# Kernel tuning notes

Measured on AMD Instinct MI355X. Metric: run time of the kernel, lower is better.

The kernel has to match this reference:

```python
import jax, jax.numpy as jnp
import numpy as np

DEPTH = 11          # tree depth
D = 1024            # input_width
H = 32              # hidden_width (leaf MLP)
O = 1024            # output_width
B = 4096            # flattened token batch
N_LEAVES = 2 ** DEPTH
N_NODES = 2 ** DEPTH - 1


def setup_inputs() -> dict:
    key = jax.random.key(0)
    ks = jax.random.split(key, 7)
    f1 = 1.0 / np.sqrt(D)
    f2 = 1.0 / np.sqrt(H)
    u = lambda k, shape, f: jax.random.uniform(k, shape, jnp.float32, -f, f)
    return {
        "x": jax.random.normal(ks[0], (B, D), jnp.float32),
        "node_weights": u(ks[1], (N_NODES, D), f1),
        "node_biases": u(ks[2], (N_NODES,), f1),   # (n_nodes,1) in torch; flattened
        "w1s": u(ks[3], (N_LEAVES, D, H), f1),
        "b1s": u(ks[4], (N_LEAVES, H), f1),
        "w2s": u(ks[5], (N_LEAVES, H, O), f2),
        "b2s": u(ks[6], (N_LEAVES, O), f2),
    }


def reference(x, node_weights, node_biases, w1s, b1s, w2s, b2s):
    # --- hard tree descent (eval_forward) ---
    nodes = jnp.zeros((x.shape[0],), jnp.int32)
    for i in range(DEPTH):  # fixed small loop over tree depth
        w = node_weights[nodes]                       # [B, D] gathered plane coeffs
        b = node_biases[nodes]                        # [B]
        score = jnp.einsum('bd,bd->b', x, w) + b      # per-sample dot product
        choice = (score >= 0).astype(jnp.int32)
        platform = 2 ** i - 1
        next_platform = 2 ** (i + 1) - 1
        nodes = (nodes - platform) * 2 + choice + next_platform
    leaves = nodes - (2 ** DEPTH - 1)                 # [B] leaf index per sample

    # --- per-sample leaf MLP with gathered weights ---
    h = jax.nn.relu(jnp.einsum('bd,bdh->bh', x, w1s[leaves]) + b1s[leaves])  # [B, H]
    out = jnp.einsum('bh,bho->bo', h, w2s[leaves]) + b2s[leaves]             # [B, O]
    return out
```

## Files before the change

kernel.cpp:

```cpp
#include <hip/hip_runtime.h>

#define DEPTH 11
#define D 1024
#define H 32
#define OW 1024
#define B 4096
#define N_LEAVES 2048
#define N_NODES 2047
#define SMAX 4
#define MAX_ITEMS 3072
#define NBLK 512
#define MAXK 6

typedef __attribute__((address_space(3))) void lds_void;
typedef const __attribute__((address_space(1))) void glb_void;

#define SB __builtin_amdgcn_sched_barrier(0)
#define WAITV(N) do { asm volatile("s_waitcnt vmcnt(" #N ")" ::: "memory"); SB; } while (0)
#define WAITLG0  do { asm volatile("s_waitcnt lgkmcnt(0)" ::: "memory"); SB; } while (0)
#define BARRIER  do { WAITLG0; __builtin_amdgcn_s_barrier(); \
                      asm volatile("" ::: "memory"); SB; } while (0)

__global__ __launch_bounds__(256) void descent_kernel(
    const float* __restrict__ x, const float* __restrict__ nw,
    const float* __restrict__ nb, int* __restrict__ leaf,
    int* __restrict__ rnk, int* __restrict__ count)
{
    int lane = threadIdx.x & 63;
    int wv   = threadIdx.x >> 6;
    int samp = blockIdx.x * 4 + wv;

    const float4* xp = (const float4*)(x + (size_t)samp * D);
    float4 xf[4];
#pragma unroll
    for (int k = 0; k < 4; k++) xf[k] = xp[lane + 64 * k];

    int node = 0;
#pragma unroll
    for (int i = 0; i < DEPTH; i++) {
        const float4* wp = (const float4*)(nw + (size_t)node * D);
        double s = 0.0;
#pragma unroll
        for (int k = 0; k < 4; k++) {
            float4 wf = wp[lane + 64 * k];
            s += (double)xf[k].x * (double)wf.x;
            s += (double)xf[k].y * (double)wf.y;
            s += (double)xf[k].z * (double)wf.z;
            s += (double)xf[k].w * (double)wf.w;
        }
#pragma unroll
        for (int m = 32; m >= 1; m >>= 1) s += __shfl_xor(s, m, 64);
        double score = s + (double)nb[node];
        int choice = (score >= 0.0) ? 1 : 0;
        node = 2 * node + 1 + choice;
    }
    int lf = node - N_NODES;
    if (lane == 0) {
        leaf[samp] = lf;
        rnk[samp]  = atomicAdd(&count[lf], 1);
    }
}

__global__ __launch_bounds__(256) void scan_kernel(
    const int* __restrict__ count, int* __restrict__ offsets)
{
    __shared__ int tot[256];
    int t = threadIdx.x;
    int c[8], s = 0;
#pragma unroll
    for (int k = 0; k < 8; k++) { c[k] = count[t * 8 + k]; s += c[k]; }
    tot[t] = s;
    __syncthreads();
    for (int off = 1; off < 256; off <<= 1) {
        int v = (t >= off) ? tot[t - off] : 0;
        __syncthreads();
        tot[t] += v;
        __syncthreads();
    }
    int base = (t > 0) ? tot[t - 1] : 0;
#pragma unroll
    for (int k = 0; k < 8; k++) { offsets[t * 8 + k] = base; base += c[k]; }
}

__global__ __launch_bounds__(256) void scatter_kernel(
    const int* __restrict__ leaf, const int* __restrict__ rnk,
    const int* __restrict__ offsets, int* __restrict__ bucket)
{
    int i = blockIdx.x * 256 + threadIdx.x;
    bucket[offsets[leaf[i]] + rnk[i]] = i;
}

__global__ __launch_bounds__(256) void build_items_kernel(
    const int* __restrict__ count, int* __restrict__ items,
    int* __restrict__ nitems)
{
    int l = blockIdx.x * 256 + threadIdx.x;
    int c = count[l];
    if (c > 0) {
        int k = (c + SMAX - 1) / SMAX;
        int base = atomicAdd(nitems, k);
        for (int i = 0; i < k; i++)
            items[base + i] = l | ((i * SMAX) << 11);
    }
}

__device__ __forceinline__ void stage4(const float* src, float* dst, int lane)
{
#pragma unroll
    for (int i = 0; i < 4; i++)
        __builtin_amdgcn_global_load_lds((glb_void*)(src + i * 256 + lane * 4),
                                         (lds_void*)(dst + i * 256), 16, 0, 0);
}

__device__ __forceinline__ void stageL2g(const float* w2w, int cj, float* dst, int lane)
{
#pragma unroll
    for (int jl = 0; jl < 4; jl++)
        __builtin_amdgcn_global_load_lds(
            (glb_void*)(w2w + (size_t)(cj * 4 + jl) * OW + lane * 4),
            (lds_void*)(dst + jl * 256), 16, 0, 0);
}

__device__ __forceinline__ void stageXB(const float* x, const int* sid4,
                                        const float* b1, const float* b2,
                                        float* xsd, float* b1d, float* b2d,
                                        int wave, int lane)
{
#pragma unroll
    for (int s = 0; s < 4; s++)
        __builtin_amdgcn_global_load_lds(
            (glb_void*)(x + (size_t)sid4[s] * D + wave * 256 + lane * 4),
            (lds_void*)(xsd + s * D + wave * 256), 16, 0, 0);
    __builtin_amdgcn_global_load_lds(
        (glb_void*)(b1 + ((lane < 32) ? lane : 31)), (lds_void*)b1d, 4, 0, 0);
    __builtin_amdgcn_global_load_lds(
        (glb_void*)(b2 + wave * 256 + lane * 4), (lds_void*)b2d, 16, 0, 0);
}

__device__ __forceinline__ void l1c(const float* p, const float* xsw, int c,
                                    int lane, int dg, float4* acc)
{
#pragma unroll
    for (int u = 0; u < 4; u++) {
        float4 w = ((const float4*)p)[u * 64 + lane];
#pragma unroll
        for (int s = 0; s < 4; s++) {
            float xv = xsw[s * D + c * 32 + u * 8 + dg];
            acc[s].x += xv * w.x;
            acc[s].y += xv * w.y;
            acc[s].z += xv * w.z;
            acc[s].w += xv * w.w;
        }
    }
}

__device__ __forceinline__ void l2c(const float* p, const float (*hsv)[32], int cj,
                                    int lane, float4* o)
{
#pragma unroll
    for (int jl = 0; jl < 4; jl++) {
        float4 w = ((const float4*)p)[jl * 64 + lane];
#pragma unroll
        for (int s = 0; s < 4; s++) {
            float hv = hsv[s][cj * 4 + jl];
            o[s].x += hv * w.x;
            o[s].y += hv * w.y;
            o[s].z += hv * w.z;
            o[s].w += hv * w.w;
        }
    }
}

__global__ __launch_bounds__(256, 2) void mlp_kernel(
    const float* __restrict__ x, const float* __restrict__ w1s,
    const float* __restrict__ b1s, const float* __restrict__ w2s,
    const float* __restrict__ b2s, const int* __restrict__ offsets,
    const int* __restrict__ count, const int* __restrict__ bucket,
    const int* __restrict__ items, const int* __restrict__ nitems,
    float* __restrict__ out)
{
    __shared__ float xs[SMAX * D];
    __shared__ float wq_[4][2][1024];
    __shared__ float pl1[4][SMAX][32];
    __shared__ float hs[SMAX][32];
    __shared__ float b1l[2][4][64];
    __shared__ float b2l[2][4][256];
    __shared__ int   md_leaf[MAXK];
    __shared__ int   md_sid[MAXK][4];

    const int tid = threadIdx.x, lane = tid & 63, wave = tid >> 6;
    const int dg = lane >> 3;
    const int bid = blockIdx.x;

    int nit = nitems[0];
    if (tid < MAXK) {
        int idx = bid + tid * NBLK;
        if (idx < nit) {
            int it = items[idx];
            int l = it & (N_LEAVES - 1), st = it >> 11;
            int c = count[l] - st;
            int S = (c < SMAX) ? c : SMAX;
            int off = offsets[l] + st;
            md_leaf[tid] = l;
            for (int s = 0; s < 4; s++)
                md_sid[tid][s] = bucket[off + ((s < S) ? s : (S - 1))];
        }
    }
    __syncthreads();
    int n_my = (nit - bid + NBLK - 1) >> 9;
    if (n_my <= 0) return;
    if (n_my > MAXK) n_my = MAXK;

    float* WQ0 = &wq_[wave][0][0];
    float* WQ1 = &wq_[wave][1][0];
    const float* xsw = xs + wave * 256;

    int lc = md_leaf[0];
    {
        const float* w1w = w1s + (size_t)lc * 32768 + wave * 8192;
        stage4(w1w, WQ0, lane);
        stageXB(x, md_sid[0], b1s + lc * H, b2s + (size_t)lc * OW,
                xs, &b1l[0][wave][0], &b2l[0][wave][0], wave, lane);
        stage4(w1w + 1024, WQ1, lane);
        stage4(w1w + 1024, WQ1, lane);
    }

    for (int k = 0; k < n_my; k++) {
        const int p  = k & 1;
        const int kn = (k + 1 < n_my) ? (k + 1) : k;
        const int ln = md_leaf[kn];
        const float* w1c = w1s + (size_t)lc * 32768 + wave * 8192;
        const float* w2c = w2s + (size_t)lc * 32768 + wave * 256;
        const float* w1n = w1s + (size_t)ln * 32768 + wave * 8192;
        int sc[4];
#pragma unroll
        for (int s = 0; s < 4; s++) sc[s] = md_sid[k][s];

        float4 acc[4];
#pragma unroll
        for (int s = 0; s < 4; s++) acc[s] = make_float4(0.f, 0.f, 0.f, 0.f);

        WAITV(8);  l1c(WQ0, xsw, 0, lane, dg, acc); SB; stage4(w1c + 2 * 1024, WQ0, lane);
        WAITV(8);  l1c(WQ1, xsw, 1, lane, dg, acc); SB; stage4(w1c + 3 * 1024, WQ1, lane);
        WAITV(4);  l1c(WQ0, xsw, 2, lane, dg, acc); SB; stage4(w1c + 4 * 1024, WQ0, lane);
        WAITV(4);  l1c(WQ1, xsw, 3, lane, dg, acc); SB; stage4(w1c + 5 * 1024, WQ1, lane);
        WAITV(4);  l1c(WQ0, xsw, 4, lane, dg, acc); SB; stage4(w1c + 6 * 1024, WQ0, lane);
        WAITV(4);  l1c(WQ1, xsw, 5, lane, dg, acc); SB; stage4(w1c + 7 * 1024, WQ1, lane);
        WAITV(4);  l1c(WQ0, xsw, 6, lane, dg, acc); SB; stageL2g(w2c, 0, WQ0, lane);
        WAITV(4);  l1c(WQ1, xsw, 7, lane, dg, acc); SB; stageL2g(w2c, 1, WQ1, lane);

#pragma unroll
        for (int m = 8; m <= 32; m <<= 1)
#pragma unroll
            for (int s = 0; s < 4; s++) {
                acc[s].x += __shfl_xor(acc[s].x, m, 64);
                acc[s].y += __shfl_xor(acc[s].y, m, 64);
                acc[s].z += __shfl_xor(acc[s].z, m, 64);
                acc[s].w += __shfl_xor(acc[s].w, m, 64);
            }
        if (dg == 0) {
#pragma unroll
            for (int s = 0; s < 4; s++)
                *(float4*)&pl1[wave][s][(lane & 7) * 4] = acc[s];
        }
        BARRIER;
        if (tid < 128) {
            int s2 = tid >> 5, j2 = tid & 31;
            float sum = pl1[0][s2][j2] + pl1[1][s2][j2] + pl1[2][s2][j2] +
                        pl1[3][s2][j2] + b1l[p][tid >> 6][j2];
            hs[s2][j2] = fmaxf(sum, 0.f);
        }
        BARRIER;

        float4 o[4];
#pragma unroll
        for (int s = 0; s < 4; s++) o[s] = make_float4(0.f, 0.f, 0.f, 0.f);

        WAITV(4);  l2c(WQ0, hs, 0, lane, o); SB; stageL2g(w2c, 2, WQ0, lane);
        WAITV(4);  l2c(WQ1, hs, 1, lane, o); SB; stageL2g(w2c, 3, WQ1, lane);
        WAITV(4);  l2c(WQ0, hs, 2, lane, o); SB; stageL2g(w2c, 4, WQ0, lane);
        WAITV(4);  l2c(WQ1, hs, 3, lane, o); SB; stageL2g(w2c, 5, WQ1, lane);
        WAITV(4);  l2c(WQ0, hs, 4, lane, o); SB; stageL2g(w2c, 6, WQ0, lane);
        WAITV(4);  l2c(WQ1, hs, 5, lane, o); SB; stageL2g(w2c, 7, WQ1, lane);
        WAITV(4);  l2c(WQ0, hs, 6, lane, o); SB;
        stage4(w1n, WQ0, lane);
        stageXB(x, md_sid[kn], b1s + ln * H, b2s + (size_t)ln * OW,
                xs, &b1l[p ^ 1][wave][0], &b2l[p ^ 1][wave][0], wave, lane);
        WAITV(10); l2c(WQ1, hs, 7, lane, o); SB;
        stage4(w1n + 1024, WQ1, lane);

        float4 bv = ((const float4*)&b2l[p][wave][0])[lane];
#pragma unroll
        for (int s = 0; s < 4; s++) {
            float4 o4;
            o4.x = o[s].x + bv.x;
            o4.y = o[s].y + bv.y;
            o4.z = o[s].z + bv.z;
            o4.w = o[s].w + bv.w;
            *(float4*)(out + (size_t)sc[s] * OW + wave * 256 + lane * 4) = o4;
        }
        lc = ln;
    }
}

extern "C" void kernel_launch(void* const* d_in, const int* in_sizes, int n_in,
                              void* d_out, int out_size, void* d_ws, size_t ws_size,
                              hipStream_t stream)
{
    const float* x   = (const float*)d_in[0];
    const float* nw  = (const float*)d_in[1];
    const float* nb  = (const float*)d_in[2];
    const float* w1s = (const float*)d_in[3];
    const float* b1s = (const float*)d_in[4];
    const float* w2s = (const float*)d_in[5];
    const float* b2s = (const float*)d_in[6];
    float* out = (float*)d_out;

    int* leaf    = (int*)d_ws;
    int* rnk     = leaf + B;
    int* count   = rnk + B;
    int* offsets = count + N_LEAVES;
    int* bucket  = offsets + N_LEAVES;
    int* items   = bucket + B;
    int* nitems  = items + MAX_ITEMS;

    hipMemsetAsync(count, 0, N_LEAVES * sizeof(int), stream);
    hipMemsetAsync(nitems, 0, sizeof(int), stream);
    descent_kernel<<<B / 4, 256, 0, stream>>>(x, nw, nb, leaf, rnk, count);
    scan_kernel<<<1, 256, 0, stream>>>(count, offsets);
    scatter_kernel<<<B / 256, 256, 0, stream>>>(leaf, rnk, offsets, bucket);
    build_items_kernel<<<N_LEAVES / 256, 256, 0, stream>>>(count, items, nitems);
    mlp_kernel<<<NBLK, 256, 0, stream>>>(x, w1s, b1s, w2s, b2s,
                                         offsets, count, bucket,
                                         items, nitems, out);
}
```

Measured before the change: 129.8 us.

## Stream leaf MLP weights into registers instead of LDS staging, raise occupancy

Replaces the LDS double-buffered staging of W1/W2 tiles (global_load_lds) with direct global_load_dwordx4 into register arrays under manual vmcnt-based pipelining, and removes the per-wave weight LDS buffers. It also raises the launch bound to 3 blocks per CU and changes the work split to 768 blocks with at most 4 items each. The aim is to cut LDS traffic and ds_read latency and to increase occupancy for this memory-bound gathered-weight MLP. The cost is much higher register pressure from 24 float4 buffers, which under the new launch bound could cause spills, and the hand-counted vmcnt waits are fragile.

Measured after the change: 128.1 us. No clear change (-1.3%).

```diff
diff --git a/kernel.cpp b/kernel.cpp
--- a/kernel.cpp
+++ b/kernel.cpp
@@ -9,9 +9,10 @@
 #define N_NODES 2047
 #define SMAX 4
 #define MAX_ITEMS 3072
-#define NBLK 512
-#define MAXK 6
-
+#define NBLK 768
+#define MAXK 4
+
+typedef float f32x4 __attribute__((ext_vector_type(4)));
 typedef __attribute__((address_space(3))) void lds_void;
 typedef const __attribute__((address_space(1))) void glb_void;
 
@@ -20,6 +21,8 @@
 #define WAITLG0  do { asm volatile("s_waitcnt lgkmcnt(0)" ::: "memory"); SB; } while (0)
 #define BARRIER  do { WAITLG0; __builtin_amdgcn_s_barrier(); \
                       asm volatile("" ::: "memory"); SB; } while (0)
+#define GLOAD(dst, ptr) \
+    asm volatile("global_load_dwordx4 %0, %1, off" : "=&v"(dst) : "v"(ptr) : "memory")
 
 __global__ __launch_bounds__(256) void descent_kernel(
     const float* __restrict__ x, const float* __restrict__ nw,
@@ -104,74 +107,7 @@
     }
 }
 
-__device__ __forceinline__ void stage4(const float* src, float* dst, int lane)
-{
-#pragma unroll
-    for (int i = 0; i < 4; i++)
-        __builtin_amdgcn_global_load_lds((glb_void*)(src + i * 256 + lane * 4),
-                                         (lds_void*)(dst + i * 256), 16, 0, 0);
-}
-
-__device__ __forceinline__ void stageL2g(const float* w2w, int cj, float* dst, int lane)
-{
-#pragma unroll
-    for (int jl = 0; jl < 4; jl++)
-        __builtin_amdgcn_global_load_lds(
-            (glb_void*)(w2w + (size_t)(cj * 4 + jl) * OW + lane * 4),
-            (lds_void*)(dst + jl * 256), 16, 0, 0);
-}
-
-__device__ __forceinline__ void stageXB(const float* x, const int* sid4,
-                                        const float* b1, const float* b2,
-                                        float* xsd, float* b1d, float* b2d,
-                                        int wave, int lane)
-{
-#pragma unroll
-    for (int s = 0; s < 4; s++)
-        __builtin_amdgcn_global_load_lds(
-            (glb_void*)(x + (size_t)sid4[s] * D + wave * 256 + lane * 4),
-            (lds_void*)(xsd + s * D + wave * 256), 16, 0, 0);
-    __builtin_amdgcn_global_load_lds(
-        (glb_void*)(b1 + ((lane < 32) ? lane : 31)), (lds_void*)b1d, 4, 0, 0);
-    __builtin_amdgcn_global_load_lds(
-        (glb_void*)(b2 + wave * 256 + lane * 4), (lds_void*)b2d, 16, 0, 0);
-}
-
-__device__ __forceinline__ void l1c(const float* p, const float* xsw, int c,
-                                    int lane, int dg, float4* acc)
-{
-#pragma unroll
-    for (int u = 0; u < 4; u++) {
-        float4 w = ((const float4*)p)[u * 64 + lane];
-#pragma unroll
-        for (int s = 0; s < 4; s++) {
-            float xv = xsw[s * D + c * 32 + u * 8 + dg];
-            acc[s].x += xv * w.x;
-            acc[s].y += xv * w.y;
-            acc[s].z += xv * w.z;
-            acc[s].w += xv * w.w;
-        }
-    }
-}
-
-__device__ __forceinline__ void l2c(const float* p, const float (*hsv)[32], int cj,
-                                    int lane, float4* o)
-{
-#pragma unroll
-    for (int jl = 0; jl < 4; jl++) {
-        float4 w = ((const float4*)p)[jl * 64 + lane];
-#pragma unroll
-        for (int s = 0; s < 4; s++) {
-            float hv = hsv[s][cj * 4 + jl];
-            o[s].x += hv * w.x;
-            o[s].y += hv * w.y;
-            o[s].z += hv * w.z;
-            o[s].w += hv * w.w;
-        }
-    }
-}
-
-__global__ __launch_bounds__(256, 2) void mlp_kernel(
+__global__ __launch_bounds__(256, 3) void mlp_kernel(
     const float* __restrict__ x, const float* __restrict__ w1s,
     const float* __restrict__ b1s, const float* __restrict__ w2s,
     const float* __restrict__ b2s, const int* __restrict__ offsets,
@@ -179,17 +115,16 @@
     const int* __restrict__ items, const int* __restrict__ nitems,
     float* __restrict__ out)
 {
-    __shared__ float xs[SMAX * D];
-    __shared__ float wq_[4][2][1024];
-    __shared__ float pl1[4][SMAX][32];
-    __shared__ float hs[SMAX][32];
-    __shared__ float b1l[2][4][64];
-    __shared__ float b2l[2][4][256];
-    __shared__ int   md_leaf[MAXK];
-    __shared__ int   md_sid[MAXK][4];
+    __shared__ __align__(16) float xs[SMAX][D];
+    __shared__ __align__(16) float pl1[4][SMAX][32];
+    __shared__ __align__(16) float hs[SMAX][32];
+    __shared__ __align__(16) float b1l[2][4][64];
+    __shared__ __align__(16) float b2l[2][4][256];
+    __shared__ int md_leaf[MAXK];
+    __shared__ int md_sid[MAXK][4];
 
     const int tid = threadIdx.x, lane = tid & 63, wave = tid >> 6;
-    const int dg = lane >> 3;
+    const int dg = lane >> 3, lane4 = lane * 4;
     const int bid = blockIdx.x;
 
     int nit = nitems[0];
@@ -207,61 +142,78 @@
         }
     }
     __syncthreads();
-    int n_my = (nit - bid + NBLK - 1) >> 9;
-    if (n_my <= 0) return;
+    if (bid >= nit) return;
+    int n_my = (nit - bid + NBLK - 1) / NBLK;
     if (n_my > MAXK) n_my = MAXK;
 
-    float* WQ0 = &wq_[wave][0][0];
-    float* WQ1 = &wq_[wave][1][0];
-    const float* xsw = xs + wave * 256;
+    f32x4 w1r[2][4];
+    f32x4 w2r[16];
+
+#define L1I(base, cc, bb) do { _Pragma("unroll") \
+    for (int u = 0; u < 4; u++) \
+        GLOAD(w1r[bb][u], (base) + (cc) * 1024 + u * 256 + lane4); } while (0)
+
+#define L1C(cc, bb) do { _Pragma("unroll") \
+    for (int u = 0; u < 4; u++) { \
+        f32x4 wv_ = w1r[bb][u]; \
+        _Pragma("unroll") \
+        for (int s = 0; s < 4; s++) \
+            acc[s] += xs[s][wave * 256 + (cc) * 32 + u * 8 + dg] * wv_; } } while (0)
 
     int lc = md_leaf[0];
+    const float* w1x = w1s + (size_t)lc * 32768 + wave * 8192;
     {
-        const float* w1w = w1s + (size_t)lc * 32768 + wave * 8192;
-        stage4(w1w, WQ0, lane);
-        stageXB(x, md_sid[0], b1s + lc * H, b2s + (size_t)lc * OW,
-                xs, &b1l[0][wave][0], &b2l[0][wave][0], wave, lane);
-        stage4(w1w + 1024, WQ1, lane);
-        stage4(w1w + 1024, WQ1, lane);
+#pragma unroll
+        for (int pp = 0; pp < 4; pp++)
+            __builtin_amdgcn_global_load_lds(
+                (glb_void*)(x + (size_t)md_sid[0][pp] * D + wave * 256 + lane4),
+                (lds_void*)(&xs[pp][wave * 256]), 16, 0, 0);
+        __builtin_amdgcn_global_load_lds(
+            (glb_void*)(b1s + lc * H + ((lane < 32) ? lane : 31)),
+            (lds_void*)(&b1l[0][wave][0]), 4, 0, 0);
+        __builtin_amdgcn_global_load_lds(
+            (glb_void*)(b2s + (size_t)lc * OW + wave * 256 + lane4),
+            (lds_void*)(&b2l[0][wave][0]), 16, 0, 0);
+        L1I(w1x, 0, 0); L1I(w1x, 1, 1);
+        L1I(w1x, 0, 0); L1I(w1x, 1, 1);
     }
 
     for (int k = 0; k < n_my; k++) {
-        const int p  = k & 1;
-        const int kn = (k + 1 < n_my) ? (k + 1) : k;
+        const int p  = k & 1, pn = p ^ 1;
+        const int kn = (k + 1 < n_my) ? k + 1 : k;
         const int ln = md_leaf[kn];
-        const float* w1c = w1s + (size_t)lc * 32768 + wave * 8192;
-        const float* w2c = w2s + (size_t)lc * 32768 + wave * 256;
+        const float* w2x = w2s + (size_t)lc * 32768 + wave * 256;
         const float* w1n = w1s + (size_t)ln * 32768 + wave * 8192;
-        int sc[4];
-#pragma unroll
-        for (int s = 0; s < 4; s++) sc[s] = md_sid[k][s];
-
-        float4 acc[4];
-#pragma unroll
-        for (int s = 0; s < 4; s++) acc[s] = make_float4(0.f, 0.f, 0.f, 0.f);
-
-        WAITV(8);  l1c(WQ0, xsw, 0, lane, dg, acc); SB; stage4(w1c + 2 * 1024, WQ0, lane);
-        WAITV(8);  l1c(WQ1, xsw, 1, lane, dg, acc); SB; stage4(w1c + 3 * 1024, WQ1, lane);
-        WAITV(4);  l1c(WQ0, xsw, 2, lane, dg, acc); SB; stage4(w1c + 4 * 1024, WQ0, lane);
-        WAITV(4);  l1c(WQ1, xsw, 3, lane, dg, acc); SB; stage4(w1c + 5 * 1024, WQ1, lane);
-        WAITV(4);  l1c(WQ0, xsw, 4, lane, dg, acc); SB; stage4(w1c + 6 * 1024, WQ0, lane);
-        WAITV(4);  l1c(WQ1, xsw, 5, lane, dg, acc); SB; stage4(w1c + 7 * 1024, WQ1, lane);
-        WAITV(4);  l1c(WQ0, xsw, 6, lane, dg, acc); SB; stageL2g(w2c, 0, WQ0, lane);
-        WAITV(4);  l1c(WQ1, xsw, 7, lane, dg, acc); SB; stageL2g(w2c, 1, WQ1, lane);
+        int sidc[4];
+#pragma unroll
+        for (int s = 0; s < 4; s++) sidc[s] = md_sid[k][s];
+
+        f32x4 acc[4] = {};
+
+        WAITV(8); L1C(0, 0); L1I(w1x, 2, 0);
+        WAITV(8); L1C(1, 1); L1I(w1x, 3, 1);
+        WAITV(4); L1C(2, 0); L1I(w1x, 4, 0);
+        WAITV(4); L1C(3, 1); L1I(w1x, 5, 1);
+        WAITV(4); L1C(4, 0); L1I(w1x, 6, 0);
+        WAITV(4); L1C(5, 1); L1I(w1x, 7, 1);
+        WAITV(4); L1C(6, 0);
+#pragma unroll
+        for (int j = 0; j < 8; j++) GLOAD(w2r[j], w2x + j * 1024 + lane4);
+        WAITV(8); L1C(7, 1);
+#pragma unroll
+        for (int j = 8; j < 16; j++) GLOAD(w2r[j], w2x + j * 1024 + lane4);
 
 #pragma unroll
         for (int m = 8; m <= 32; m <<= 1)
 #pragma unroll
-            for (int s = 0; s < 4; s++) {
-                acc[s].x += __shfl_xor(acc[s].x, m, 64);
-                acc[s].y += __shfl_xor(acc[s].y, m, 64);
-                acc[s].z += __shfl_xor(acc[s].z, m, 64);
-                acc[s].w += __shfl_xor(acc[s].w, m, 64);
-            }
+            for (int s = 0; s < 4; s++)
+#pragma unroll
+                for (int e = 0; e < 4; e++)
+                    acc[s][e] += __shfl_xor(acc[s][e], m, 64);
         if (dg == 0) {
 #pragma unroll
             for (int s = 0; s < 4; s++)
-                *(float4*)&pl1[wave][s][(lane & 7) * 4] = acc[s];
+                *(f32x4*)&pl1[wave][s][(lane & 7) * 4] = acc[s];
         }
         BARRIER;
         if (tid < 128) {
@@ -272,35 +224,46 @@
         }
         BARRIER;
 
-        float4 o[4];
-#pragma unroll
-        for (int s = 0; s < 4; s++) o[s] = make_float4(0.f, 0.f, 0.f, 0.f);
-
-        WAITV(4);  l2c(WQ0, hs, 0, lane, o); SB; stageL2g(w2c, 2, WQ0, lane);
-        WAITV(4);  l2c(WQ1, hs, 1, lane, o); SB; stageL2g(w2c, 3, WQ1, lane);
-        WAITV(4);  l2c(WQ0, hs, 2, lane, o); SB; stageL2g(w2c, 4, WQ0, lane);
-        WAITV(4);  l2c(WQ1, hs, 3, lane, o); SB; stageL2g(w2c, 5, WQ1, lane);
-        WAITV(4);  l2c(WQ0, hs, 4, lane, o); SB; stageL2g(w2c, 6, WQ0, lane);
-        WAITV(4);  l2c(WQ1, hs, 5, lane, o); SB; stageL2g(w2c, 7, WQ1, lane);
-        WAITV(4);  l2c(WQ0, hs, 6, lane, o); SB;
-        stage4(w1n, WQ0, lane);
-        stageXB(x, md_sid[kn], b1s + ln * H, b2s + (size_t)ln * OW,
-                xs, &b1l[p ^ 1][wave][0], &b2l[p ^ 1][wave][0], wave, lane);
-        WAITV(10); l2c(WQ1, hs, 7, lane, o); SB;
-        stage4(w1n + 1024, WQ1, lane);
-
-        float4 bv = ((const float4*)&b2l[p][wave][0])[lane];
+        f32x4 o[4] = {};
+#pragma unroll
+        for (int jj = 0; jj < 32; jj++) {
+            if (jj == 31) { WAITV(14); } else { WAITV(15); }
+            f32x4 w = w2r[jj & 15];
+#pragma unroll
+            for (int s = 0; s < 4; s++) o[s] += hs[s][jj] * w;
+            if (jj < 16) {
+                GLOAD(w2r[jj & 15], w2x + (jj + 16) * 1024 + lane4);
+            } else if (jj < 20) {
+                const int pp = jj - 16;
+                __builtin_amdgcn_global_load_lds(
+                    (glb_void*)(x + (size_t)md_sid[kn][pp] * D + wave * 256 + lane4),
+                    (lds_void*)(&xs[pp][wave * 256]), 16, 0, 0);
+            } else if (jj == 20) {
+                __builtin_amdgcn_global_load_lds(
+                    (glb_void*)(b1s + ln * H + ((lane < 32) ? lane : 31)),
+                    (lds_void*)(&b1l[pn][wave][0]), 4, 0, 0);
+            } else if (jj == 21) {
+                __builtin_amdgcn_global_load_lds(
+                    (glb_void*)(b2s + (size_t)ln * OW + wave * 256 + lane4),
+                    (lds_void*)(&b2l[pn][wave][0]), 16, 0, 0);
+            } else if (jj < 26) {
+                GLOAD(w1r[0][jj - 22], w1n + (jj - 22) * 256 + lane4);
+            } else if (jj < 30) {
+                GLOAD(w1r[1][jj - 26], w1n + 1024 + (jj - 26) * 256 + lane4);
+            }
+        }
+
+        f32x4 bv = *(const f32x4*)&b2l[p][wave][lane4];
 #pragma unroll
         for (int s = 0; s < 4; s++) {
-            float4 o4;
-            o4.x = o[s].x + bv.x;
-            o4.y = o[s].y + bv.y;
-            o4.z = o[s].z + bv.z;
-            o4.w = o[s].w + bv.w;
-            *(float4*)(out + (size_t)sc[s] * OW + wave * 256 + lane * 4) = o4;
+            f32x4 ov = o[s] + bv;
+            *(f32x4*)(out + (size_t)sidc[s] * OW + wave * 256 + lane4) = ov;
         }
         lc = ln;
-    }
+        w1x = w1n;
+    }
+#undef L1I
+#undef L1C
 }
 
 extern "C" void kernel_launch(void* const* d_in, const int* in_sizes, int n_in,
```
